# Performance work log

Hardware: AMD Instinct MI355X
Metric: run time of the kernel (lower is better)

Reference implementation:

```python
import jax, jax.numpy as jnp
import numpy as np

PATCH = 32      # patch_size
OUT = 224       # output_size
K = 9           # num_patches (3x3 grid)
GRID = 3


def _srm_kernel():
    # filter1 + filter2 + filter3 combined (as in SRMConv._get_srm_kernels)
    f = np.array([[-1., 3., -1.], [3., -8., 3.], [-1., 3., -1.]], dtype=np.float32)
    k = np.zeros((3, 3, 3, 3), dtype=np.float32)
    for i in range(3):
        k[i, i] = f
    return jnp.asarray(k)


def setup_inputs() -> dict:
    key = jax.random.key(0)
    x = jax.random.uniform(key, (16, 3, 1024, 1024), dtype=jnp.float32)
    return {"x": x, "srm_kernel": _srm_kernel()}


def reference(x, srm_kernel):
    B, C, H, W = x.shape
    nh, nw = H // PATCH, W // PATCH
    # [N, B, C, P, P], N patches in row-major (i, j) order to match the loop
    p = x.reshape(B, C, nh, PATCH, nw, PATCH).transpose(2, 4, 0, 1, 3, 5)
    p = p.reshape(nh * nw, B, C, PATCH, PATCH)

    dx = jnp.abs(p[..., 1:] - p[..., :-1])
    dy = jnp.abs(p[..., 1:, :] - p[..., :-1, :])
    ax = (1, 2, 3, 4)  # stats over the whole batch, as in the original .item() scoring
    grad_mean = (dx.mean(axis=ax) + dy.mean(axis=ax)) * 0.5
    grad_var = (jnp.var(dx, axis=ax, ddof=1) + jnp.var(dy, axis=ax, ddof=1)) * 0.5
    score = grad_mean * grad_var                      # [N]

    order = jnp.argsort(score)                        # ascending, like np.argsort
    rich = p[order[-K:]]                              # [9, B, C, P, P]
    poor = p[order[:K]]

    def reconstruct(ps):
        # 3x3 grid of PATCH x PATCH patches -> [B, C, 3P, 3P]
        g = ps.reshape(GRID, GRID, B, C, PATCH, PATCH)
        return g.transpose(2, 3, 0, 4, 1, 5).reshape(B, C, GRID * PATCH, GRID * PATCH)

    def upsample(img):
        # bilinear, align_corners=False (half-pixel centers), upsampling so antialias is a no-op
        return jax.image.resize(img, (B, C, OUT, OUT), method='bilinear')

    def srm(img):
        return jax.lax.conv_general_dilated(
            img, srm_kernel, window_strides=(1, 1), padding=((1, 1), (1, 1)),
            dimension_numbers=('NCHW', 'OIHW', 'NCHW'))

    rich_srm = srm(upsample(reconstruct(rich)))       # [B, 3, 224, 224]
    poor_srm = srm(upsample(reconstruct(poor)))
    return jnp.stack([rich_srm, poor_srm])            # [2, B, 3, 224, 224]
```

## Files before the change

### kernel.cpp

```cpp
#include <hip/hip_runtime.h>


#define NSLICE 48
#define IMG    1048576
#define TILE   8

__global__ __launch_bounds__(256) void k_score(const float* __restrict__ x,
                                               double* __restrict__ part) {
  const int ph = blockIdx.x;
  const int s  = blockIdx.y;
  const int t  = threadIdx.x;
  const float* base = x + (size_t)s * IMG + (size_t)ph * 32768 + 4 * t;

  double s1x = 0.0, s2x = 0.0, s1y = 0.0, s2y = 0.0;
  const bool has_d3 = (t & 7) != 7;

#define LD(r) (*(const float4*)(base + (size_t)(r) * 1024))
#define DX(v) { float nx = __shfl_down((v).x, 1);                              \
    float d0 = fabsf((v).y-(v).x), d1 = fabsf((v).z-(v).y), d2 = fabsf((v).w-(v).z); \
    s1x += d0; s2x += (double)d0*d0;                                           \
    s1x += d1; s2x += (double)d1*d1;                                           \
    s1x += d2; s2x += (double)d2*d2;                                           \
    if (has_d3) { float d3 = fabsf(nx-(v).w); s1x += d3; s2x += (double)d3*d3; } }
#define DY(a,b) { float e0 = fabsf((b).x-(a).x), e1 = fabsf((b).y-(a).y),      \
                        e2 = fabsf((b).z-(a).z), e3 = fabsf((b).w-(a).w);      \
    s1y += e0; s2y += (double)e0*e0;                                           \
    s1y += e1; s2y += (double)e1*e1;                                           \
    s1y += e2; s2y += (double)e2*e2;                                           \
    s1y += e3; s2y += (double)e3*e3; }

  float4 v0 = LD(0);
  for (int r = 0; r < 32; r += 4) {
    float4 v1 = LD(r + 1);
    float4 v2 = LD(r + 2);
    float4 v3 = LD(r + 3);
    float4 v4;
    const bool more = (r + 4 < 32);
    if (more) v4 = LD(r + 4);
    DX(v0); DX(v1); DX(v2); DX(v3);
    DY(v0, v1); DY(v1, v2); DY(v2, v3);
    if (more) { DY(v3, v4); v0 = v4; }
  }
#undef LD
#undef DX
#undef DY

#pragma unroll
  for (int off = 4; off > 0; off >>= 1) {
    s1x += __shfl_down(s1x, off, 8);
    s2x += __shfl_down(s2x, off, 8);
    s1y += __shfl_down(s1y, off, 8);
    s2y += __shfl_down(s2y, off, 8);
  }
  if ((t & 7) == 0) {
    const int p = ph * 32 + (t >> 3);
    part[(size_t)(0 * NSLICE + s) * 1024 + p] = s1x;
    part[(size_t)(1 * NSLICE + s) * 1024 + p] = s2x;
    part[(size_t)(2 * NSLICE + s) * 1024 + p] = s1y;
    part[(size_t)(3 * NSLICE + s) * 1024 + p] = s2y;
  }
}

__global__ __launch_bounds__(256) void k_finalize(const double* __restrict__ part,
                                                  double* __restrict__ scores) {
  const int p = blockIdx.x * 256 + threadIdx.x;
  double S[4];
#pragma unroll
  for (int q = 0; q < 4; ++q) {
    const double* b = part + (size_t)q * NSLICE * 1024 + p;
    double a = 0.0;
    for (int s = 0; s < NSLICE; ++s) a += b[(size_t)s * 1024];
    S[q] = a;
  }
  const double N = 47616.0;
  double mx = S[0] / N, my = S[2] / N;
  double vx = (S[1] - S[0] * S[0] / N) / (N - 1.0);
  double vy = (S[3] - S[2] * S[2] / N) / (N - 1.0);
  scores[p] = 0.25 * (mx + my) * (vx + vy);
}

__global__ __launch_bounds__(256) void k_rank(const double* __restrict__ scores,
                                              int* __restrict__ sel) {
  __shared__ double sc[1024];
  const int t = threadIdx.x;
  for (int i = t; i < 1024; i += 256) sc[i] = scores[i];
  __syncthreads();

  const int c = blockIdx.x * 32 + (t >> 3);
  const double mine = sc[c];
  int rank = 0;
  for (int j = (t & 7); j < 1024; j += 8) {
    double vj = sc[j];
    rank += (vj < mine) || (vj == mine && j < c);
  }
#pragma unroll
  for (int off = 4; off > 0; off >>= 1) rank += __shfl_down(rank, off, 8);
  if ((t & 7) == 0) {
    if (rank < 9)          sel[9 + rank]    = c;
    else if (rank >= 1015) sel[rank - 1015] = c;
  }
}

__global__ __launch_bounds__(256) void k_output(const float* __restrict__ x,
                                                const int* __restrict__ sel,
                                                float* __restrict__ out) {
  const int ty  = blockIdx.x;
  const int blk = blockIdx.y;
  const int set = blk / 48;
  const int bc  = blk % 48;
  const int y0  = ty * TILE;

  __shared__ int   i0t[224];
  __shared__ float frt[224];
  __shared__ float R[6][97];
  __shared__ float H[6][224];
  __shared__ float U[10][224];
  __shared__ int   selm[9];
  const int t = threadIdx.x;

  if (t < 9) selm[t] = sel[set * 9 + t];
  if (t < 224) {
    int num = 3 * t - 2;
    int i0, fr7;
    if (num < 0) { i0 = 0; fr7 = 0; }
    else {
      i0 = num / 7; fr7 = num - i0 * 7;
      if (i0 >= 95) { i0 = 95; fr7 = 0; }
    }
    i0t[t] = i0;
    frt[t] = (float)fr7 * (1.0f / 7.0f);
  }
  __syncthreads();

  const int Ylo   = max(y0 - 1, 0);
  const int Yhi   = min(y0 + TILE, 223);
  const int sy_lo = i0t[Ylo];
  const int sy_hi = min(i0t[Yhi] + 1, 95);
  const int nrows = sy_hi - sy_lo + 1;

  const float* src = x + (size_t)bc * IMG;
  for (int idx = t; idx < nrows * 96; idx += 256) {
    int ry = idx / 96, xx = idx - ry * 96;
    int sy = sy_lo + ry;
    int gr = sy >> 5, i = sy & 31;
    int gc = xx >> 5, j = xx & 31;
    int pidx = selm[gr * 3 + gc];
    R[ry][xx] = src[(size_t)((pidx >> 5) * 32 + i) * 1024 + (pidx & 31) * 32 + j];
  }
  __syncthreads();

  for (int idx = t; idx < nrows * 224; idx += 256) {
    int r = idx / 224, X = idx - r * 224;
    int ix0 = i0t[X], ix1 = min(ix0 + 1, 95);
    float fx = frt[X];
    float a = R[r][ix0], b = R[r][ix1];
    H[r][X] = a + fx * (b - a);
  }
  __syncthreads();

  for (int idx = t; idx < 10 * 224; idx += 256) {
    int yy = idx / 224, X = idx - yy * 224;
    int Y = y0 - 1 + yy;
    if ((unsigned)Y < 224u) {
      int a = i0t[Y] - sy_lo;
      int b = min(i0t[Y] + 1, 95) - sy_lo;
      float fy = frt[Y];
      float h0 = H[a][X], h1 = H[b][X];
      U[yy][X] = h0 + fy * (h1 - h0);
    }
  }
  __syncthreads();

  const float F[3][3] = {{-1.f, 3.f, -1.f}, {3.f, -8.f, 3.f}, {-1.f, 3.f, -1.f}};
  float* o = out + (size_t)blk * (224 * 224);
  for (int idx = t; idx < TILE * 224; idx += 256) {
    int yy = idx / 224;
    int xx = idx - yy * 224;
    int y  = y0 + yy;
    float acc = 0.f;
#pragma unroll
    for (int dy = 0; dy < 3; ++dy) {
      int Y = y + dy - 1;
      if ((unsigned)Y >= 224u) continue;
      const float* Ur = U[yy + dy];
#pragma unroll
      for (int dx = 0; dx < 3; ++dx) {
        int X = xx + dx - 1;
        if ((unsigned)X >= 224u) continue;
        acc += F[dy][dx] * Ur[X];
      }
    }
    o[(size_t)y * 224 + xx] = acc;
  }
}

extern "C" void kernel_launch(void* const* d_in, const int* in_sizes, int n_in,
                              void* d_out, int out_size, void* d_ws, size_t ws_size,
                              hipStream_t stream) {
  const float* x = (const float*)d_in[0];
  float* out = (float*)d_out;

  double* part   = (double*)d_ws;
  double* scores = (double*)((char*)d_ws + 1572864);
  int*    sel    = (int*)((char*)d_ws + 1581056);

  k_score   <<<dim3(32, 48), 256, 0, stream>>>(x, part);
  k_finalize<<<4, 256, 0, stream>>>(part, scores);
  k_rank    <<<32, 256, 0, stream>>>(scores, sel);
  k_output  <<<dim3(28, 96), 256, 0, stream>>>(x, sel, out);
}
```

Measured before the change: 76.61 us.

## Fuse finalize into rank kernel, batch float partial sums, unroll score loads

```diff
diff --git a/kernel.cpp b/kernel.cpp
--- a/kernel.cpp
+++ b/kernel.cpp
@@ -17,29 +17,27 @@
 
 #define LD(r) (*(const float4*)(base + (size_t)(r) * 1024))
 #define DX(v) { float nx = __shfl_down((v).x, 1);                              \
-    float d0 = fabsf((v).y-(v).x), d1 = fabsf((v).z-(v).y), d2 = fabsf((v).w-(v).z); \
-    s1x += d0; s2x += (double)d0*d0;                                           \
-    s1x += d1; s2x += (double)d1*d1;                                           \
-    s1x += d2; s2x += (double)d2*d2;                                           \
-    if (has_d3) { float d3 = fabsf(nx-(v).w); s1x += d3; s2x += (double)d3*d3; } }
+    float d0 = fabsf((v).y-(v).x), d1 = fabsf((v).z-(v).y),                    \
+          d2 = fabsf((v).w-(v).z);                                             \
+    float d3 = has_d3 ? fabsf(nx-(v).w) : 0.f;                                 \
+    s1x += (double)((d0+d1)+(d2+d3));                                          \
+    s2x += (double)((d0*d0+d1*d1)+(d2*d2+d3*d3)); }
 #define DY(a,b) { float e0 = fabsf((b).x-(a).x), e1 = fabsf((b).y-(a).y),      \
                         e2 = fabsf((b).z-(a).z), e3 = fabsf((b).w-(a).w);      \
-    s1y += e0; s2y += (double)e0*e0;                                           \
-    s1y += e1; s2y += (double)e1*e1;                                           \
-    s1y += e2; s2y += (double)e2*e2;                                           \
-    s1y += e3; s2y += (double)e3*e3; }
+    s1y += (double)((e0+e1)+(e2+e3));                                          \
+    s2y += (double)((e0*e0+e1*e1)+(e2*e2+e3*e3)); }
 
   float4 v0 = LD(0);
-  for (int r = 0; r < 32; r += 4) {
-    float4 v1 = LD(r + 1);
-    float4 v2 = LD(r + 2);
-    float4 v3 = LD(r + 3);
-    float4 v4;
-    const bool more = (r + 4 < 32);
-    if (more) v4 = LD(r + 4);
-    DX(v0); DX(v1); DX(v2); DX(v3);
-    DY(v0, v1); DY(v1, v2); DY(v2, v3);
-    if (more) { DY(v3, v4); v0 = v4; }
+  for (int r = 0; r < 32; r += 8) {
+    float4 w1 = LD(r + 1), w2 = LD(r + 2), w3 = LD(r + 3), w4 = LD(r + 4);
+    float4 w5 = LD(r + 5), w6 = LD(r + 6), w7 = LD(r + 7);
+    float4 w8;
+    const bool more = (r + 8 < 32);
+    if (more) w8 = LD(r + 8);
+    DX(v0); DX(w1); DX(w2); DX(w3); DX(w4); DX(w5); DX(w6); DX(w7);
+    DY(v0, w1); DY(w1, w2); DY(w2, w3); DY(w3, w4);
+    DY(w4, w5); DY(w5, w6); DY(w6, w7);
+    if (more) { DY(w7, w8); v0 = w8; }
   }
 #undef LD
 #undef DX
@@ -61,29 +59,34 @@
   }
 }
 
-__global__ __launch_bounds__(256) void k_finalize(const double* __restrict__ part,
-                                                  double* __restrict__ scores) {
-  const int p = blockIdx.x * 256 + threadIdx.x;
-  double S[4];
-#pragma unroll
-  for (int q = 0; q < 4; ++q) {
-    const double* b = part + (size_t)q * NSLICE * 1024 + p;
-    double a = 0.0;
-    for (int s = 0; s < NSLICE; ++s) a += b[(size_t)s * 1024];
-    S[q] = a;
-  }
-  const double N = 47616.0;
-  double mx = S[0] / N, my = S[2] / N;
-  double vx = (S[1] - S[0] * S[0] / N) / (N - 1.0);
-  double vy = (S[3] - S[2] * S[2] / N) / (N - 1.0);
-  scores[p] = 0.25 * (mx + my) * (vx + vy);
-}
-
-__global__ __launch_bounds__(256) void k_rank(const double* __restrict__ scores,
-                                              int* __restrict__ sel) {
+__global__ __launch_bounds__(256) void k_rankall(const double* __restrict__ part,
+                                                 int* __restrict__ sel) {
   __shared__ double sc[1024];
   const int t = threadIdx.x;
-  for (int i = t; i < 1024; i += 256) sc[i] = scores[i];
+
+  double S[4][4];
+#pragma unroll
+  for (int pi = 0; pi < 4; ++pi)
+#pragma unroll
+    for (int q = 0; q < 4; ++q) S[pi][q] = 0.0;
+
+  for (int s = 0; s < NSLICE; ++s) {
+#pragma unroll
+    for (int q = 0; q < 4; ++q) {
+      const double* b = part + (size_t)(q * NSLICE + s) * 1024 + t;
+#pragma unroll
+      for (int pi = 0; pi < 4; ++pi) S[pi][q] += b[pi * 256];
+    }
+  }
+
+  const double N = 47616.0;
+#pragma unroll
+  for (int pi = 0; pi < 4; ++pi) {
+    double mx = S[pi][0] / N, my = S[pi][2] / N;
+    double vx = (S[pi][1] - S[pi][0] * S[pi][0] / N) / (N - 1.0);
+    double vy = (S[pi][3] - S[pi][2] * S[pi][2] / N) / (N - 1.0);
+    sc[t + pi * 256] = 0.25 * (mx + my) * (vx + vy);
+  }
   __syncthreads();
 
   const int c = blockIdx.x * 32 + (t >> 3);
@@ -200,12 +203,10 @@
   const float* x = (const float*)d_in[0];
   float* out = (float*)d_out;
 
-  double* part   = (double*)d_ws;
-  double* scores = (double*)((char*)d_ws + 1572864);
-  int*    sel    = (int*)((char*)d_ws + 1581056);
-
-  k_score   <<<dim3(32, 48), 256, 0, stream>>>(x, part);
-  k_finalize<<<4, 256, 0, stream>>>(part, scores);
-  k_rank    <<<32, 256, 0, stream>>>(scores, sel);
-  k_output  <<<dim3(28, 96), 256, 0, stream>>>(x, sel, out);
-}
+  double* part = (double*)d_ws;
+  int*    sel  = (int*)((char*)d_ws + 1572864);
+
+  k_score  <<<dim3(32, 48), 256, 0, stream>>>(x, part);
+  k_rankall<<<32, 256, 0, stream>>>(part, sel);
+  k_output <<<dim3(28, 96), 256, 0, stream>>>(x, sel, out);
+}
```

After: 107.8 us. +40.8%, slower.
